# Kernel optimization log

Hardware: AMD Instinct MI355X
Metric: run time of the kernel (lower is better)

Reference implementation:

```python
import math
import jax, jax.numpy as jnp
import numpy as np

DIM = 512
HEADS = 8
B, N = 4, 2048


def _linear_params(key, d_in, d_out):
    # torch nn.Linear default init: U(-1/sqrt(d_in), 1/sqrt(d_in))
    k1, k2 = jax.random.split(key)
    bound = 1.0 / math.sqrt(d_in)
    W = jax.random.uniform(k1, (d_out, d_in), minval=-bound, maxval=bound, dtype=jnp.float32)
    b = jax.random.uniform(k2, (d_out,), minval=-bound, maxval=bound, dtype=jnp.float32)
    return W, b


def setup_inputs() -> dict:
    key = jax.random.key(0)
    kq, kv, km, k1, k2, k3, k4 = jax.random.split(key, 7)
    Q = jax.random.normal(kq, (B, N, DIM), dtype=jnp.float32)
    V = jax.random.normal(kv, (B, N, DIM), dtype=jnp.float32)
    mask = jax.random.bernoulli(km, 0.9, (B, N))  # bool [B, Nk]
    Wq, bq = _linear_params(k1, DIM, DIM)
    Wk, bk = _linear_params(k2, DIM, DIM)
    Wv, bv = _linear_params(k3, DIM, DIM)
    Wo, bo = _linear_params(k4, DIM, DIM)
    return {"Q": Q, "V": V, "mask": mask,
            "Wq": Wq, "bq": bq, "Wk": Wk, "bk": bk,
            "Wv": Wv, "bv": bv, "Wo": Wo, "bo": bo}


def reference(Q, V, mask, Wq, bq, Wk, bk, Wv, bv, Wo, bo):
    Bb, Nq, _ = Q.shape
    dv = Wq.shape[0]
    h = HEADS
    d = dv // h
    q = Q @ Wq.T + bq          # [B, Nq, dv]
    k = V @ Wk.T + bk          # [B, Nk, dv]
    v = V @ Wv.T + bv          # [B, Nk, dv]
    # split heads: torch.cat(split(dim_split, dim=2), dim=0) == head-major stacking
    qh = q.reshape(Bb, Nq, h, d).transpose(2, 0, 1, 3)   # [h, B, Nq, d]
    kh = k.reshape(Bb, -1, h, d).transpose(2, 0, 1, 3)   # [h, B, Nk, d]
    vh = v.reshape(Bb, -1, h, d).transpose(2, 0, 1, 3)   # [h, B, Nk, d]
    # NOTE: original scales by sqrt(Q.shape[-1]) AFTER projection == sqrt(dim_V)
    logits = jnp.einsum('hbqd,hbkd->hbqk', qh, kh) / math.sqrt(dv)
    logits = jnp.where(mask[None, :, None, :], logits, jnp.float32(-100.0))
    A = jax.nn.softmax(logits, axis=-1)
    Oh = qh + jnp.einsum('hbqk,hbkd->hbqd', A, vh)       # residual inside attention
    O = Oh.transpose(1, 2, 0, 3).reshape(Bb, Nq, dv)     # merge heads
    return O + jax.nn.relu(O @ Wo.T + bo)
```

## Files before the change

kernel.cpp:

```cpp
#include <hip/hip_runtime.h>


typedef __attribute__((ext_vector_type(8))) __bf16 bf16x8;
typedef __attribute__((ext_vector_type(4))) float f32x4;

#define DEV static __device__ __forceinline__

constexpr int DIMC = 512;
constexpr int NTOK = 2048;
constexpr int BB   = 4;
constexpr int MTOK = BB * NTOK;
constexpr float SCALE2 = 0.04419417382415922f * 1.4426950408889634f;

DEV unsigned short f2b(float f) {
  unsigned u = __float_as_uint(f);
  u = (u + 0x7FFFu + ((u >> 16) & 1u)) >> 16;
  return (unsigned short)u;
}
DEV float b2f(unsigned short b) { return __uint_as_float(((unsigned)b) << 16); }

DEV unsigned cvtpk(float a, float b) {
  unsigned r;
  asm("v_cvt_pk_bf16_f32 %0, %1, %2" : "=v"(r) : "v"(a), "v"(b));
  return r;
}

DEV bf16x8 pack8(unsigned d0, unsigned d1, unsigned d2, unsigned d3) {
  union { unsigned u[4]; bf16x8 v; } t;
  t.u[0] = d0; t.u[1] = d1; t.u[2] = d2; t.u[3] = d3;
  return t.v;
}

DEV void async_cp16(const void* src, void* dst) {
  __builtin_amdgcn_global_load_lds(
      (const __attribute__((address_space(1))) void*)(src),
      (__attribute__((address_space(3))) void*)(dst), 16, 0, 0);
}

__global__ void cvt_all(const float* __restrict__ Wq, const float* __restrict__ Wk,
                        const float* __restrict__ Wv, const float* __restrict__ Wo,
                        unsigned short* __restrict__ Wqb, unsigned short* __restrict__ Wkb,
                        unsigned short* __restrict__ Wvb, unsigned short* __restrict__ Wob,
                        const unsigned char* __restrict__ mask, int* __restrict__ flag) {
  if (blockIdx.x == 4096) {
    int any = 0;
    for (int i = threadIdx.x; i < BB * NTOK; i += blockDim.x)
      if ((i & 3) == 1 && mask[i]) any = 1;
    if (any) atomicOr(flag, 1);
    return;
  }
  int i = blockIdx.x * blockDim.x + threadIdx.x;
  int wsel = i >> 16, off = i & 65535;
  const float* s = (wsel == 0) ? Wq : (wsel == 1) ? Wk : (wsel == 2) ? Wv : Wo;
  unsigned short* d = (wsel == 0) ? Wqb : (wsel == 1) ? Wkb : (wsel == 2) ? Wvb : Wob;
  float4 v = reinterpret_cast<const float4*>(s)[off];
  ushort4 o;
  o.x = f2b(v.x); o.y = f2b(v.y); o.z = f2b(v.z); o.w = f2b(v.w);
  reinterpret_cast<ushort4*>(d)[off] = o;
}

__global__ __launch_bounds__(256) void proj_gemm(
    const float* __restrict__ Qf, const float* __restrict__ Vf,
    const unsigned short* __restrict__ Wqb, const unsigned short* __restrict__ Wkb,
    const unsigned short* __restrict__ Wvb,
    const float* __restrict__ bq, const float* __restrict__ bk,
    const float* __restrict__ bv,
    unsigned short* __restrict__ qbf, unsigned short* __restrict__ kbf,
    unsigned short* __restrict__ vtb) {
  __shared__ union {
    struct { float A[2][4096]; unsigned short B[2][4096]; } s;
    unsigned short LT[128 * 136];
  } lds;

  const int region = blockIdx.z;
  const float* Af = (region == 0) ? Qf : Vf;
  const unsigned short* W = (region == 0) ? Wqb : (region == 1) ? Wkb : Wvb;
  const float* bias = (region == 0) ? bq : (region == 1) ? bk : bv;

  const int tid = threadIdx.x;
  const int lane = tid & 63;
  const int w = tid >> 6;
  const int r = lane & 15, g = lane >> 4;
  const int rowB = blockIdx.x * 128;
  const int colB = blockIdx.y * 128;
  const int rw = (w >> 1) * 64, cw = (w & 1) * 64;

  auto stageA = [&](float* dst, int kk) {
#pragma unroll
    for (int i = 0; i < 4; ++i) {
      int off = i * 4096 + tid * 16;
      int row = off >> 7;
      int c = ((off >> 4) & 7) ^ (row & 7);
      async_cp16(Af + (size_t)(rowB + row) * DIMC + kk + c * 4, (char*)dst + off);
    }
  };
  auto stageB = [&](unsigned short* dst, int kk) {
#pragma unroll
    for (int i = 0; i < 2; ++i) {
      int off = i * 4096 + tid * 16;
      int row = off >> 6;
      int c = ((off >> 4) & 3) ^ (row & 3);
      async_cp16(W + (size_t)(colB + row) * DIMC + kk + c * 8, (char*)dst + off);
    }
  };

  f32x4 acc[4][4];
#pragma unroll
  for (int i = 0; i < 4; ++i)
#pragma unroll
    for (int j = 0; j < 4; ++j) acc[i][j] = f32x4{0.f, 0.f, 0.f, 0.f};

  stageA(lds.s.A[0], 0);
  stageB(lds.s.B[0], 0);
  __syncthreads();

  int cur = 0;
  for (int kk = 0; kk < DIMC; kk += 32) {
    if (kk + 32 < DIMC) {
      stageA(lds.s.A[cur ^ 1], kk + 32);
      stageB(lds.s.B[cur ^ 1], kk + 32);
    }
    const char* ap = (const char*)lds.s.A[cur];
    const char* bp = (const char*)lds.s.B[cur];
    bf16x8 af[4], bw[4];
#pragma unroll
    for (int i = 0; i < 4; ++i) {
      int row = rw + i * 16 + r;
      f32x4 lo = *reinterpret_cast<const f32x4*>(
          ap + row * 128 + (((2 * g) ^ (row & 7)) << 4));
      f32x4 hi = *reinterpret_cast<const f32x4*>(
          ap + row * 128 + (((2 * g + 1) ^ (row & 7)) << 4));
      af[i] = pack8(cvtpk(lo[0], lo[1]), cvtpk(lo[2], lo[3]),
                    cvtpk(hi[0], hi[1]), cvtpk(hi[2], hi[3]));
    }
#pragma unroll
    for (int j = 0; j < 4; ++j) {
      int row = cw + j * 16 + r;
      bw[j] = *reinterpret_cast<const bf16x8*>(bp + row * 64 + ((g ^ (row & 3)) * 16));
    }
    __builtin_amdgcn_s_setprio(1);
#pragma unroll
    for (int i = 0; i < 4; ++i)
#pragma unroll
      for (int j = 0; j < 4; ++j)
        acc[i][j] = __builtin_amdgcn_mfma_f32_16x16x32_bf16(af[i], bw[j],
                                                            acc[i][j], 0, 0, 0);
    __builtin_amdgcn_s_setprio(0);
    __syncthreads();
    cur ^= 1;
  }

  if (region != 2) {
    const float sc = (region == 1) ? SCALE2 : 1.0f;
    unsigned short* dst = (region == 1) ? kbf : qbf;
#pragma unroll
    for (int i = 0; i < 4; ++i)
#pragma unroll
      for (int j = 0; j < 4; ++j) {
        int n = colB + cw + j * 16 + r;
        float bn = bias[n];
#pragma unroll
        for (int q = 0; q < 4; ++q) {
          int m = rowB + rw + i * 16 + g * 4 + q;
          dst[(size_t)m * DIMC + n] = f2b((acc[i][j][q] + bn) * sc);
        }
      }
  } else {
#pragma unroll
    for (int i = 0; i < 4; ++i)
#pragma unroll
      for (int j = 0; j < 4; ++j) {
        int nl = cw + j * 16 + r;
        float bn = bias[colB + nl];
        int tl = rw + i * 16 + g * 4;
        ushort4 o;
        o.x = f2b(acc[i][j][0] + bn);
        o.y = f2b(acc[i][j][1] + bn);
        o.z = f2b(acc[i][j][2] + bn);
        o.w = f2b(acc[i][j][3] + bn);
        *reinterpret_cast<ushort4*>(&lds.LT[nl * 136 + tl]) = o;
      }
    __syncthreads();
    int bidx = rowB >> 11, t0 = rowB & 2047;
#pragma unroll
    for (int rd = 0; rd < 8; ++rd) {
      int idx = rd * 256 + tid;
      int dv = idx >> 4, ch = idx & 15;
      int gdv = colB + dv, h = gdv >> 6, dd = gdv & 63;
      ushort4 v0 = *reinterpret_cast<const ushort4*>(&lds.LT[dv * 136 + ch * 8]);
      ushort4 v1 = *reinterpret_cast<const ushort4*>(&lds.LT[dv * 136 + ch * 8 + 4]);
      unsigned short* dst = vtb + (size_t)((bidx * 8 + h) * 64 + dd) * NTOK + t0 + ch * 8;
      reinterpret_cast<ushort4*>(dst)[0] = v0;
      reinterpret_cast<ushort4*>(dst)[1] = v1;
    }
  }
}

__global__ __launch_bounds__(256) void out_gemm(
    const float* __restrict__ Of32, const unsigned short* __restrict__ W,
    const float* __restrict__ bias, float* __restrict__ outf) {
  __shared__ struct { float A[2][2048]; unsigned short B[2][4096]; } lds;

  const int tid = threadIdx.x;
  const int lane = tid & 63;
  const int w = tid >> 6;
  const int r = lane & 15, g = lane >> 4;
  const int rowB = blockIdx.x * 64;
  const int colB = blockIdx.y * 128;
  const int rw = (w >> 1) * 32, cw = (w & 1) * 64;

  auto stageA = [&](float* dst, int kk) {
    int off = tid * 16;
#pragma unroll
    for (int i = 0; i < 2; ++i) {
      int o2 = off + i * 4096;
      int row = o2 >> 7;
      int c = ((o2 >> 4) & 7) ^ (row & 7);
      async_cp16(Of32 + (size_t)(rowB + row) * DIMC + kk + c * 4, (char*)dst + o2);
    }
  };
  auto stageB = [&](unsigned short* dst, int kk) {
#pragma unroll
    for (int i = 0; i < 2; ++i) {
      int off = i * 4096 + tid * 16;
      int row = off >> 6;
      int c = ((off >> 4) & 3) ^ (row & 3);
      async_cp16(W + (size_t)(colB + row) * DIMC + kk + c * 8, (char*)dst + off);
    }
  };

  f32x4 acc[2][4];
#pragma unroll
  for (int i = 0; i < 2; ++i)
#pragma unroll
    for (int j = 0; j < 4; ++j) acc[i][j] = f32x4{0.f, 0.f, 0.f, 0.f};

  stageA(lds.A[0], 0);
  stageB(lds.B[0], 0);
  __syncthreads();

  int cur = 0;
  for (int kk = 0; kk < DIMC; kk += 32) {
    if (kk + 32 < DIMC) {
      stageA(lds.A[cur ^ 1], kk + 32);
      stageB(lds.B[cur ^ 1], kk + 32);
    }
    const char* ap = (const char*)lds.A[cur];
    const char* bp = (const char*)lds.B[cur];
    bf16x8 af[2], bw[4];
#pragma unroll
    for (int i = 0; i < 2; ++i) {
      int row = rw + i * 16 + r;
      f32x4 lo = *reinterpret_cast<const f32x4*>(
          ap + row * 128 + (((2 * g) ^ (row & 7)) << 4));
      f32x4 hi = *reinterpret_cast<const f32x4*>(
          ap + row * 128 + (((2 * g + 1) ^ (row & 7)) << 4));
      af[i] = pack8(cvtpk(lo[0], lo[1]), cvtpk(lo[2], lo[3]),
                    cvtpk(hi[0], hi[1]), cvtpk(hi[2], hi[3]));
    }
#pragma unroll
    for (int j = 0; j < 4; ++j) {
      int row = cw + j * 16 + r;
      bw[j] = *reinterpret_cast<const bf16x8*>(bp + row * 64 + ((g ^ (row & 3)) * 16));
    }
    __builtin_amdgcn_s_setprio(1);
#pragma unroll
    for (int i = 0; i < 2; ++i)
#pragma unroll
      for (int j = 0; j < 4; ++j)
        acc[i][j] = __builtin_amdgcn_mfma_f32_16x16x32_bf16(af[i], bw[j],
                                                            acc[i][j], 0, 0, 0);
    __builtin_amdgcn_s_setprio(0);
    __syncthreads();
    cur ^= 1;
  }

#pragma unroll
  for (int i = 0; i < 2; ++i)
#pragma unroll
    for (int j = 0; j < 4; ++j) {
      int n = colB + cw + j * 16 + r;
      float bn = bias[n];
#pragma unroll
      for (int q = 0; q < 4; ++q) {
        int m = rowB + rw + i * 16 + g * 4 + q;
        float val = acc[i][j][q] + bn;
        outf[(size_t)m * DIMC + n] = Of32[(size_t)m * DIMC + n] + fmaxf(val, 0.f);
      }
    }
}

__global__ __launch_bounds__(512, 4) void attn_kernel(
    const unsigned short* __restrict__ qb, const unsigned short* __restrict__ kb,
    const unsigned short* __restrict__ vt, const unsigned char* __restrict__ mask8,
    const int* __restrict__ flagp, float* __restrict__ Of32) {
  __shared__ unsigned short Kt[2][2][64 * 64];
  __shared__ unsigned short Vt[2][2][64 * 64];
  __shared__ float MaskAdd[NTOK];

  const int tid = threadIdx.x;
  const int lane = tid & 63;
  const int w = tid >> 6;
  const int kg = w >> 2;
  const int wq = w & 3;
  const int r = lane & 15, g = lane >> 4;
  const int bh = blockIdx.x, b = bh >> 3, h = bh & 7;
  const int q0 = blockIdx.y * 128 + wq * 32;
  const size_t rowbase = (size_t)b * NTOK;
  const int flag = *flagp;
  const unsigned* mask32 = (const unsigned*)mask8;

  for (int i = tid; i < NTOK; i += 512) {
    unsigned v = flag ? (unsigned)mask8[b * NTOK + i] : mask32[b * NTOK + i];
    MaskAdd[i] = v ? 0.f : -16384.f;
  }

  bf16x8 aq0[2], aq1[2];
#pragma unroll
  for (int ks = 0; ks < 2; ++ks) {
    aq0[ks] = *reinterpret_cast<const bf16x8*>(
        qb + (rowbase + q0 + r) * DIMC + h * 64 + ks * 32 + g * 8);
    aq1[ks] = *reinterpret_cast<const bf16x8*>(
        qb + (rowbase + q0 + 16 + r) * DIMC + h * 64 + ks * 32 + g * 8);
  }

  const unsigned short* kgb = kb + rowbase * DIMC + h * 64;
  const unsigned short* vgb = vt + (size_t)bh * 64 * NTOK;

  auto stageK = [&](int pb, int tile, int kt) {
    int off = tid * 16;
    int row = off >> 7;
    int s16 = ((off >> 4) & 7) ^ (row & 7);
    int ff = row >> 4, gg = (row >> 2) & 3, j = row & 3;
    int tok = 8 * gg + 4 * (ff & 1) + 32 * (ff >> 1) + j;
    async_cp16(kgb + (size_t)(kt + tok) * DIMC + (s16 << 3),
               (char*)&Kt[pb][tile][0] + off);
  };
  auto stageV = [&](int pb, int tile, int kt) {
    int off = tid * 16;
    int row = off >> 7;
    int s16 = ((off >> 4) & 7) ^ (row & 7);
    async_cp16(vgb + (size_t)row * NTOK + kt + (s16 << 3),
               (char*)&Vt[pb][tile][0] + off);
  };
  auto stagePair = [&](int pb, int p) {
    stageK(pb, 0, p * 128);
    stageK(pb, 1, p * 128 + 64);
    stageV(pb, 0, p * 128);
    stageV(pb, 1, p * 128 + 64);
  };

  stagePair(0, 0);
  __syncthreads();

  float lrun0 = 0.f, lrun1 = 0.f;
  f32x4 oacc0[4], oacc1[4];
#pragma unroll
  for (int f = 0; f < 4; ++f) {
    oacc0[f] = f32x4{0.f, 0.f, 0.f, 0.f};
    oacc1[f] = f32x4{0.f, 0.f, 0.f, 0.f};
  }

  const int swz = (r & 7) << 4;

  auto softmax_pa = [&](f32x4 (&s)[4], float& lr, bf16x8 (&pa)[2]) {
#pragma unroll
    for (int f = 0; f < 4; ++f)
#pragma unroll
      for (int j = 0; j < 4; ++j) s[f][j] = __builtin_exp2f(s[f][j]);
    float sf[4];
#pragma unroll
    for (int f = 0; f < 4; ++f)
      sf[f] = (s[f][0] + s[f][1]) + (s[f][2] + s[f][3]);
    lr += (sf[0] + sf[1]) + (sf[2] + sf[3]);
#pragma unroll
    for (int ks = 0; ks < 2; ++ks)
      pa[ks] = pack8(cvtpk(s[2 * ks][0], s[2 * ks][1]),
                     cvtpk(s[2 * ks][2], s[2 * ks][3]),
                     cvtpk(s[2 * ks + 1][0], s[2 * ks + 1][1]),
                     cvtpk(s[2 * ks + 1][2], s[2 * ks + 1][3]));
  };

  int cur = 0;
  for (int p = 0; p < NTOK / 128; ++p) {
    if (p + 1 < NTOK / 128) stagePair(cur ^ 1, p + 1);

    const int kt = p * 128 + kg * 64;

    f32x4 s0[4], s1[4];
#pragma unroll
    for (int f = 0; f < 4; ++f) {
      int tb = kt + 8 * g + 4 * (f & 1) + 32 * (f >> 1);
      f32x4 mc = *reinterpret_cast<const f32x4*>(&MaskAdd[tb]);
      s0[f] = mc;
      s1[f] = mc;
    }
    const unsigned char* kp = (const unsigned char*)&Kt[cur][kg][0];
    __builtin_amdgcn_s_setprio(1);
#pragma unroll
    for (int ks = 0; ks < 2; ++ks)
#pragma unroll
      for (int f = 0; f < 4; ++f) {
        bf16x8 kf = *reinterpret_cast<const bf16x8*>(
            kp + (f * 16 + r) * 128 + ((ks * 64 + g * 16) ^ swz));
        s0[f] = __builtin_amdgcn_mfma_f32_16x16x32_bf16(kf, aq0[ks], s0[f], 0, 0, 0);
        s1[f] = __builtin_amdgcn_mfma_f32_16x16x32_bf16(kf, aq1[ks], s1[f], 0, 0, 0);
      }
    __builtin_amdgcn_s_setprio(0);

    bf16x8 pa0[2], pa1[2];
    softmax_pa(s0, lrun0, pa0);
    softmax_pa(s1, lrun1, pa1);

    const unsigned char* vp = (const unsigned char*)&Vt[cur][kg][0];
    __builtin_amdgcn_s_setprio(1);
#pragma unroll
    for (int ks = 0; ks < 2; ++ks)
#pragma unroll
      for (int f = 0; f < 4; ++f) {
        bf16x8 vf = *reinterpret_cast<const bf16x8*>(
            vp + (f * 16 + r) * 128 + ((ks * 64 + g * 16) ^ swz));
        oacc0[f] = __builtin_amdgcn_mfma_f32_16x16x32_bf16(pa0[ks], vf, oacc0[f], 0, 0, 0);
        oacc1[f] = __builtin_amdgcn_mfma_f32_16x16x32_bf16(pa1[ks], vf, oacc1[f], 0, 0, 0);
      }
    __builtin_amdgcn_s_setprio(0);

    __syncthreads();
    cur ^= 1;
  }

  lrun0 += __shfl_xor(lrun0, 16);
  lrun0 += __shfl_xor(lrun0, 32);
  lrun1 += __shfl_xor(lrun1, 16);
  lrun1 += __shfl_xor(lrun1, 32);

  f32x4* cb4 = (f32x4*)&Kt[0][0][0];
  float* cl = (float*)&Vt[0][0][0];
  if (kg == 1) {
#pragma unroll
    for (int f = 0; f < 4; ++f) {
      cb4[wq * 512 + f * 64 + lane] = oacc0[f];
      cb4[wq * 512 + (4 + f) * 64 + lane] = oacc1[f];
    }
    if (g == 0) {
      cl[wq * 32 + r] = lrun0;
      cl[wq * 32 + 16 + r] = lrun1;
    }
  }
  __syncthreads();
  if (kg == 0) {
#pragma unroll
    for (int f = 0; f < 4; ++f) {
      oacc0[f] += cb4[wq * 512 + f * 64 + lane];
      oacc1[f] += cb4[wq * 512 + (4 + f) * 64 + lane];
    }
    lrun0 += cl[wq * 32 + r];
    lrun1 += cl[wq * 32 + 16 + r];

    auto epilogue = [&](float lr, f32x4 (&oa)[4], int qoff) {
#pragma unroll
      for (int j = 0; j < 4; ++j) {
        float linv = 1.0f / __shfl(lr, (lane & 48) | (g * 4 + j));
        int row = q0 + qoff + g * 4 + j;
#pragma unroll
        for (int f = 0; f < 4; ++f) {
          int col = h * 64 + f * 16 + r;
          size_t idx = (rowbase + row) * DIMC + col;
          Of32[idx] = b2f(qb[idx]) + oa[f][j] * linv;
        }
      }
    };
    epilogue(lrun0, oacc0, 0);
    epilogue(lrun1, oacc1, 16);
  }
}

extern "C" void kernel_launch(void* const* d_in, const int* in_sizes, int n_in,
                              void* d_out, int out_size, void* d_ws, size_t ws_size,
                              hipStream_t stream) {
  const float* Q  = (const float*)d_in[0];
  const float* V  = (const float*)d_in[1];
  const unsigned char* mask = (const unsigned char*)d_in[2];
  const float* Wq = (const float*)d_in[3];
  const float* bq = (const float*)d_in[4];
  const float* Wk = (const float*)d_in[5];
  const float* bk = (const float*)d_in[6];
  const float* Wv = (const float*)d_in[7];
  const float* bv = (const float*)d_in[8];
  const float* Wo = (const float*)d_in[9];
  const float* bo = (const float*)d_in[10];

  char* ws = (char*)d_ws;
  size_t off = 0;
  auto alloc = [&](size_t bytes) -> void* {
    void* p = ws + off;
    off += (bytes + 255) & ~(size_t)255;
    return p;
  };
  int* flag = (int*)alloc(4);
  unsigned short* Wqb = (unsigned short*)alloc((size_t)DIMC * DIMC * 2);
  unsigned short* Wkb = (unsigned short*)alloc((size_t)DIMC * DIMC * 2);
  unsigned short* Wvb = (unsigned short*)alloc((size_t)DIMC * DIMC * 2);
  unsigned short* Wob = (unsigned short*)alloc((size_t)DIMC * DIMC * 2);
  unsigned short* qbf = (unsigned short*)alloc((size_t)MTOK * DIMC * 2);
  unsigned short* kbf = (unsigned short*)alloc((size_t)MTOK * DIMC * 2);
  unsigned short* vtb = (unsigned short*)alloc((size_t)MTOK * DIMC * 2);
  float* Of32 = (float*)alloc((size_t)MTOK * DIMC * 4);

  hipMemsetAsync(flag, 0, 4, stream);

  cvt_all<<<4097, 256, 0, stream>>>(Wq, Wk, Wv, Wo, Wqb, Wkb, Wvb, Wob,
                                    mask, flag);

  proj_gemm<<<dim3(64, 4, 3), 256, 0, stream>>>(
      Q, V, Wqb, Wkb, Wvb, bq, bk, bv, qbf, kbf, vtb);

  attn_kernel<<<dim3(BB * 8, NTOK / 128), 512, 0, stream>>>(
      qbf, kbf, vtb, mask, flag, Of32);

  out_gemm<<<dim3(128, 4), 256, 0, stream>>>(
      Of32, Wob, bo, (float*)d_out);
}
```

Measured before the change: 117.6 us.

## Halve attention block to 4 waves, each computing 64 query rows

The attention kernel now launches 256 threads per block instead of 512. Each wave handles four 16-row query subtiles instead of two, so every K/V fragment read from LDS is reused across 64 query rows, and each thread issues two async copies per tile. This cuts LDS traffic per MFMA and sync overhead, but roughly doubles accumulator and score registers per wave and lowers the waves available per block to hide latency.

```diff
diff --git a/kernel.cpp b/kernel.cpp
--- a/kernel.cpp
+++ b/kernel.cpp
@@ -290,7 +290,7 @@
     }
 }
 
-__global__ __launch_bounds__(512, 4) void attn_kernel(
+__global__ __launch_bounds__(256, 2) void attn_kernel(
     const unsigned short* __restrict__ qb, const unsigned short* __restrict__ kb,
     const unsigned short* __restrict__ vt, const unsigned char* __restrict__ mask8,
     const int* __restrict__ flagp, float* __restrict__ Of32) {
@@ -301,47 +301,52 @@
   const int tid = threadIdx.x;
   const int lane = tid & 63;
   const int w = tid >> 6;
-  const int kg = w >> 2;
-  const int wq = w & 3;
+  const int kg = w >> 1;
+  const int wq = w & 1;
   const int r = lane & 15, g = lane >> 4;
   const int bh = blockIdx.x, b = bh >> 3, h = bh & 7;
-  const int q0 = blockIdx.y * 128 + wq * 32;
+  const int q0 = blockIdx.y * 128 + wq * 64;
   const size_t rowbase = (size_t)b * NTOK;
   const int flag = *flagp;
   const unsigned* mask32 = (const unsigned*)mask8;
 
-  for (int i = tid; i < NTOK; i += 512) {
+  for (int i = tid; i < NTOK; i += 256) {
     unsigned v = flag ? (unsigned)mask8[b * NTOK + i] : mask32[b * NTOK + i];
     MaskAdd[i] = v ? 0.f : -16384.f;
   }
 
-  bf16x8 aq0[2], aq1[2];
-#pragma unroll
-  for (int ks = 0; ks < 2; ++ks) {
-    aq0[ks] = *reinterpret_cast<const bf16x8*>(
-        qb + (rowbase + q0 + r) * DIMC + h * 64 + ks * 32 + g * 8);
-    aq1[ks] = *reinterpret_cast<const bf16x8*>(
-        qb + (rowbase + q0 + 16 + r) * DIMC + h * 64 + ks * 32 + g * 8);
-  }
+  bf16x8 aq[4][2];
+#pragma unroll
+  for (int sub = 0; sub < 4; ++sub)
+#pragma unroll
+    for (int ks = 0; ks < 2; ++ks)
+      aq[sub][ks] = *reinterpret_cast<const bf16x8*>(
+          qb + (rowbase + q0 + sub * 16 + r) * DIMC + h * 64 + ks * 32 + g * 8);
 
   const unsigned short* kgb = kb + rowbase * DIMC + h * 64;
   const unsigned short* vgb = vt + (size_t)bh * 64 * NTOK;
 
   auto stageK = [&](int pb, int tile, int kt) {
-    int off = tid * 16;
-    int row = off >> 7;
-    int s16 = ((off >> 4) & 7) ^ (row & 7);
-    int ff = row >> 4, gg = (row >> 2) & 3, j = row & 3;
-    int tok = 8 * gg + 4 * (ff & 1) + 32 * (ff >> 1) + j;
-    async_cp16(kgb + (size_t)(kt + tok) * DIMC + (s16 << 3),
-               (char*)&Kt[pb][tile][0] + off);
+#pragma unroll
+    for (int i = 0; i < 2; ++i) {
+      int off = i * 4096 + tid * 16;
+      int row = off >> 7;
+      int s16 = ((off >> 4) & 7) ^ (row & 7);
+      int ff = row >> 4, gg = (row >> 2) & 3, j = row & 3;
+      int tok = 8 * gg + 4 * (ff & 1) + 32 * (ff >> 1) + j;
+      async_cp16(kgb + (size_t)(kt + tok) * DIMC + (s16 << 3),
+                 (char*)&Kt[pb][tile][0] + off);
+    }
   };
   auto stageV = [&](int pb, int tile, int kt) {
-    int off = tid * 16;
-    int row = off >> 7;
-    int s16 = ((off >> 4) & 7) ^ (row & 7);
-    async_cp16(vgb + (size_t)row * NTOK + kt + (s16 << 3),
-               (char*)&Vt[pb][tile][0] + off);
+#pragma unroll
+    for (int i = 0; i < 2; ++i) {
+      int off = i * 4096 + tid * 16;
+      int row = off >> 7;
+      int s16 = ((off >> 4) & 7) ^ (row & 7);
+      async_cp16(vgb + (size_t)row * NTOK + kt + (s16 << 3),
+                 (char*)&Vt[pb][tile][0] + off);
+    }
   };
   auto stagePair = [&](int pb, int p) {
     stageK(pb, 0, p * 128);
@@ -353,33 +358,14 @@
   stagePair(0, 0);
   __syncthreads();
 
-  float lrun0 = 0.f, lrun1 = 0.f;
-  f32x4 oacc0[4], oacc1[4];
-#pragma unroll
-  for (int f = 0; f < 4; ++f) {
-    oacc0[f] = f32x4{0.f, 0.f, 0.f, 0.f};
-    oacc1[f] = f32x4{0.f, 0.f, 0.f, 0.f};
-  }
+  float lrun[4] = {0.f, 0.f, 0.f, 0.f};
+  f32x4 oacc[4][4];
+#pragma unroll
+  for (int sub = 0; sub < 4; ++sub)
+#pragma unroll
+    for (int f = 0; f < 4; ++f) oacc[sub][f] = f32x4{0.f, 0.f, 0.f, 0.f};
 
   const int swz = (r & 7) << 4;
-
-  auto softmax_pa = [&](f32x4 (&s)[4], float& lr, bf16x8 (&pa)[2]) {
-#pragma unroll
-    for (int f = 0; f < 4; ++f)
-#pragma unroll
-      for (int j = 0; j < 4; ++j) s[f][j] = __builtin_exp2f(s[f][j]);
-    float sf[4];
-#pragma unroll
-    for (int f = 0; f < 4; ++f)
-      sf[f] = (s[f][0] + s[f][1]) + (s[f][2] + s[f][3]);
-    lr += (sf[0] + sf[1]) + (sf[2] + sf[3]);
-#pragma unroll
-    for (int ks = 0; ks < 2; ++ks)
-      pa[ks] = pack8(cvtpk(s[2 * ks][0], s[2 * ks][1]),
-                     cvtpk(s[2 * ks][2], s[2 * ks][3]),
-                     cvtpk(s[2 * ks + 1][0], s[2 * ks + 1][1]),
-                     cvtpk(s[2 * ks + 1][2], s[2 * ks + 1][3]));
-  };
 
   int cur = 0;
   for (int p = 0; p < NTOK / 128; ++p) {
@@ -387,13 +373,13 @@
 
     const int kt = p * 128 + kg * 64;
 
-    f32x4 s0[4], s1[4];
+    f32x4 s[4][4];
 #pragma unroll
     for (int f = 0; f < 4; ++f) {
       int tb = kt + 8 * g + 4 * (f & 1) + 32 * (f >> 1);
       f32x4 mc = *reinterpret_cast<const f32x4*>(&MaskAdd[tb]);
-      s0[f] = mc;
-      s1[f] = mc;
+#pragma unroll
+      for (int sub = 0; sub < 4; ++sub) s[sub][f] = mc;
     }
     const unsigned char* kp = (const unsigned char*)&Kt[cur][kg][0];
     __builtin_amdgcn_s_setprio(1);
@@ -403,14 +389,32 @@
       for (int f = 0; f < 4; ++f) {
         bf16x8 kf = *reinterpret_cast<const bf16x8*>(
             kp + (f * 16 + r) * 128 + ((ks * 64 + g * 16) ^ swz));
-        s0[f] = __builtin_amdgcn_mfma_f32_16x16x32_bf16(kf, aq0[ks], s0[f], 0, 0, 0);
-        s1[f] = __builtin_amdgcn_mfma_f32_16x16x32_bf16(kf, aq1[ks], s1[f], 0, 0, 0);
+#pragma unroll
+        for (int sub = 0; sub < 4; ++sub)
+          s[sub][f] = __builtin_amdgcn_mfma_f32_16x16x32_bf16(
+              kf, aq[sub][ks], s[sub][f], 0, 0, 0);
       }
     __builtin_amdgcn_s_setprio(0);
 
-    bf16x8 pa0[2], pa1[2];
-    softmax_pa(s0, lrun0, pa0);
-    softmax_pa(s1, lrun1, pa1);
+    bf16x8 pa[4][2];
+#pragma unroll
+    for (int sub = 0; sub < 4; ++sub) {
+#pragma unroll
+      for (int f = 0; f < 4; ++f)
+#pragma unroll
+        for (int j = 0; j < 4; ++j) s[sub][f][j] = __builtin_exp2f(s[sub][f][j]);
+      float sf[4];
+#pragma unroll
+      for (int f = 0; f < 4; ++f)
+        sf[f] = (s[sub][f][0] + s[sub][f][1]) + (s[sub][f][2] + s[sub][f][3]);
+      lrun[sub] += (sf[0] + sf[1]) + (sf[2] + sf[3]);
+#pragma unroll
+      for (int ks = 0; ks < 2; ++ks)
+        pa[sub][ks] = pack8(cvtpk(s[sub][2 * ks][0], s[sub][2 * ks][1]),
+                            cvtpk(s[sub][2 * ks][2], s[sub][2 * ks][3]),
+                            cvtpk(s[sub][2 * ks + 1][0], s[sub][2 * ks + 1][1]),
+                            cvtpk(s[sub][2 * ks + 1][2], s[sub][2 * ks + 1][3]));
+    }
 
     const unsigned char* vp = (const unsigned char*)&Vt[cur][kg][0];
     __builtin_amdgcn_s_setprio(1);
@@ -420,8 +424,10 @@
       for (int f = 0; f < 4; ++f) {
         bf16x8 vf = *reinterpret_cast<const bf16x8*>(
             vp + (f * 16 + r) * 128 + ((ks * 64 + g * 16) ^ swz));
-        oacc0[f] = __builtin_amdgcn_mfma_f32_16x16x32_bf16(pa0[ks], vf, oacc0[f], 0, 0, 0);
-        oacc1[f] = __builtin_amdgcn_mfma_f32_16x16x32_bf16(pa1[ks], vf, oacc1[f], 0, 0, 0);
+#pragma unroll
+        for (int sub = 0; sub < 4; ++sub)
+          oacc[sub][f] = __builtin_amdgcn_mfma_f32_16x16x32_bf16(
+              pa[sub][ks], vf, oacc[sub][f], 0, 0, 0);
       }
     __builtin_amdgcn_s_setprio(0);
 
@@ -429,49 +435,48 @@
     cur ^= 1;
   }
 
-  lrun0 += __shfl_xor(lrun0, 16);
-  lrun0 += __shfl_xor(lrun0, 32);
-  lrun1 += __shfl_xor(lrun1, 16);
-  lrun1 += __shfl_xor(lrun1, 32);
+#pragma unroll
+  for (int sub = 0; sub < 4; ++sub) {
+    lrun[sub] += __shfl_xor(lrun[sub], 16);
+    lrun[sub] += __shfl_xor(lrun[sub], 32);
+  }
 
   f32x4* cb4 = (f32x4*)&Kt[0][0][0];
   float* cl = (float*)&Vt[0][0][0];
   if (kg == 1) {
 #pragma unroll
-    for (int f = 0; f < 4; ++f) {
-      cb4[wq * 512 + f * 64 + lane] = oacc0[f];
-      cb4[wq * 512 + (4 + f) * 64 + lane] = oacc1[f];
-    }
+    for (int sub = 0; sub < 4; ++sub)
+#pragma unroll
+      for (int f = 0; f < 4; ++f)
+        cb4[((wq * 4 + sub) * 4 + f) * 64 + lane] = oacc[sub][f];
     if (g == 0) {
-      cl[wq * 32 + r] = lrun0;
-      cl[wq * 32 + 16 + r] = lrun1;
+#pragma unroll
+      for (int sub = 0; sub < 4; ++sub) cl[(wq * 4 + sub) * 16 + r] = lrun[sub];
     }
   }
   __syncthreads();
   if (kg == 0) {
 #pragma unroll
-    for (int f = 0; f < 4; ++f) {
-      oacc0[f] += cb4[wq * 512 + f * 64 + lane];
-      oacc1[f] += cb4[wq * 512 + (4 + f) * 64 + lane];
-    }
-    lrun0 += cl[wq * 32 + r];
-    lrun1 += cl[wq * 32 + 16 + r];
-
-    auto epilogue = [&](float lr, f32x4 (&oa)[4], int qoff) {
+    for (int sub = 0; sub < 4; ++sub) {
+#pragma unroll
+      for (int f = 0; f < 4; ++f)
+        oacc[sub][f] += cb4[((wq * 4 + sub) * 4 + f) * 64 + lane];
+      lrun[sub] += cl[(wq * 4 + sub) * 16 + r];
+    }
+
+#pragma unroll
+    for (int sub = 0; sub < 4; ++sub)
 #pragma unroll
       for (int j = 0; j < 4; ++j) {
-        float linv = 1.0f / __shfl(lr, (lane & 48) | (g * 4 + j));
-        int row = q0 + qoff + g * 4 + j;
+        float linv = 1.0f / __shfl(lrun[sub], (lane & 48) | (g * 4 + j));
+        int row = q0 + sub * 16 + g * 4 + j;
 #pragma unroll
         for (int f = 0; f < 4; ++f) {
           int col = h * 64 + f * 16 + r;
           size_t idx = (rowbase + row) * DIMC + col;
-          Of32[idx] = b2f(qb[idx]) + oa[f][j] * linv;
+          Of32[idx] = b2f(qb[idx]) + oacc[sub][f][j] * linv;
         }
       }
-    };
-    epilogue(lrun0, oacc0, 0);
-    epilogue(lrun1, oacc1, 16);
   }
 }
 
@@ -515,7 +520,7 @@
   proj_gemm<<<dim3(64, 4, 3), 256, 0, stream>>>(
       Q, V, Wqb, Wkb, Wvb, bq, bk, bv, qbf, kbf, vtb);
 
-  attn_kernel<<<dim3(BB * 8, NTOK / 128), 512, 0, stream>>>(
+  attn_kernel<<<dim3(BB * 8, NTOK / 128), 256, 0, stream>>>(
       qbf, kbf, vtb, mask, flag, Of32);
 
   out_gemm<<<dim3(128, 4), 256, 0, stream>>>(
```

After: 120.4 us. +2.4%, slower.

## Fuse K/V projections sharing the V tile and store attention output as bf16

Applied to the files above, without the earlier changes.

The projection GEMM now computes K and V together in one block, so the fp32 V activation tile is loaded and converted to bf16 once instead of twice. The grid shrinks from three regions to two. The attention output intermediate is now stored in bf16 instead of fp32, which halves its write and read traffic and removes the fp32-to-bf16 conversion in the output GEMM's A path. In exchange, the fused K/V blocks carry twice the accumulators and extra LDS, which may lower occupancy and leave the grid unbalanced. The residual added in the final output also loses precision from the bf16 rounding.

```diff
diff --git a/kernel.cpp b/kernel.cpp
--- a/kernel.cpp
+++ b/kernel.cpp
@@ -68,14 +68,12 @@
     unsigned short* __restrict__ qbf, unsigned short* __restrict__ kbf,
     unsigned short* __restrict__ vtb) {
   __shared__ union {
-    struct { float A[2][4096]; unsigned short B[2][4096]; } s;
+    struct { float A[2][4096]; unsigned short Bk[2][4096]; unsigned short Bv[2][4096]; } s;
     unsigned short LT[128 * 136];
   } lds;
 
   const int region = blockIdx.z;
   const float* Af = (region == 0) ? Qf : Vf;
-  const unsigned short* W = (region == 0) ? Wqb : (region == 1) ? Wkb : Wvb;
-  const float* bias = (region == 0) ? bq : (region == 1) ? bk : bv;
 
   const int tid = threadIdx.x;
   const int lane = tid & 63;
@@ -94,7 +92,7 @@
       async_cp16(Af + (size_t)(rowB + row) * DIMC + kk + c * 4, (char*)dst + off);
     }
   };
-  auto stageB = [&](unsigned short* dst, int kk) {
+  auto stageB = [&](unsigned short* dst, const unsigned short* W, int kk) {
 #pragma unroll
     for (int i = 0; i < 2; ++i) {
       int off = i * 4096 + tid * 16;
@@ -104,25 +102,31 @@
     }
   };
 
-  f32x4 acc[4][4];
+  f32x4 acck[4][4], accv[4][4];
 #pragma unroll
   for (int i = 0; i < 4; ++i)
 #pragma unroll
-    for (int j = 0; j < 4; ++j) acc[i][j] = f32x4{0.f, 0.f, 0.f, 0.f};
+    for (int j = 0; j < 4; ++j) {
+      acck[i][j] = f32x4{0.f, 0.f, 0.f, 0.f};
+      accv[i][j] = f32x4{0.f, 0.f, 0.f, 0.f};
+    }
 
   stageA(lds.s.A[0], 0);
-  stageB(lds.s.B[0], 0);
+  stageB(lds.s.Bk[0], (region == 0) ? Wqb : Wkb, 0);
+  if (region == 1) stageB(lds.s.Bv[0], Wvb, 0);
   __syncthreads();
 
   int cur = 0;
   for (int kk = 0; kk < DIMC; kk += 32) {
     if (kk + 32 < DIMC) {
       stageA(lds.s.A[cur ^ 1], kk + 32);
-      stageB(lds.s.B[cur ^ 1], kk + 32);
+      stageB(lds.s.Bk[cur ^ 1], (region == 0) ? Wqb : Wkb, kk + 32);
+      if (region == 1) stageB(lds.s.Bv[cur ^ 1], Wvb, kk + 32);
     }
     const char* ap = (const char*)lds.s.A[cur];
-    const char* bp = (const char*)lds.s.B[cur];
-    bf16x8 af[4], bw[4];
+    const char* bpk = (const char*)lds.s.Bk[cur];
+    const char* bpv = (const char*)lds.s.Bv[cur];
+    bf16x8 af[4], bwk[4];
 #pragma unroll
     for (int i = 0; i < 4; ++i) {
       int row = rw + i * 16 + r;
@@ -136,48 +140,74 @@
 #pragma unroll
     for (int j = 0; j < 4; ++j) {
       int row = cw + j * 16 + r;
-      bw[j] = *reinterpret_cast<const bf16x8*>(bp + row * 64 + ((g ^ (row & 3)) * 16));
+      bwk[j] = *reinterpret_cast<const bf16x8*>(bpk + row * 64 + ((g ^ (row & 3)) * 16));
     }
     __builtin_amdgcn_s_setprio(1);
 #pragma unroll
     for (int i = 0; i < 4; ++i)
 #pragma unroll
       for (int j = 0; j < 4; ++j)
-        acc[i][j] = __builtin_amdgcn_mfma_f32_16x16x32_bf16(af[i], bw[j],
-                                                            acc[i][j], 0, 0, 0);
+        acck[i][j] = __builtin_amdgcn_mfma_f32_16x16x32_bf16(af[i], bwk[j],
+                                                             acck[i][j], 0, 0, 0);
     __builtin_amdgcn_s_setprio(0);
+    if (region == 1) {
+      bf16x8 bwv[4];
+#pragma unroll
+      for (int j = 0; j < 4; ++j) {
+        int row = cw + j * 16 + r;
+        bwv[j] = *reinterpret_cast<const bf16x8*>(bpv + row * 64 + ((g ^ (row & 3)) * 16));
+      }
+      __builtin_amdgcn_s_setprio(1);
+#pragma unroll
+      for (int i = 0; i < 4; ++i)
+#pragma unroll
+        for (int j = 0; j < 4; ++j)
+          accv[i][j] = __builtin_amdgcn_mfma_f32_16x16x32_bf16(af[i], bwv[j],
+                                                               accv[i][j], 0, 0, 0);
+      __builtin_amdgcn_s_setprio(0);
+    }
     __syncthreads();
     cur ^= 1;
   }
 
-  if (region != 2) {
-    const float sc = (region == 1) ? SCALE2 : 1.0f;
-    unsigned short* dst = (region == 1) ? kbf : qbf;
+  if (region == 0) {
 #pragma unroll
     for (int i = 0; i < 4; ++i)
 #pragma unroll
       for (int j = 0; j < 4; ++j) {
         int n = colB + cw + j * 16 + r;
-        float bn = bias[n];
+        float bn = bq[n];
 #pragma unroll
         for (int q = 0; q < 4; ++q) {
           int m = rowB + rw + i * 16 + g * 4 + q;
-          dst[(size_t)m * DIMC + n] = f2b((acc[i][j][q] + bn) * sc);
+          qbf[(size_t)m * DIMC + n] = f2b(acck[i][j][q] + bn);
         }
       }
   } else {
+#pragma unroll
+    for (int i = 0; i < 4; ++i)
+#pragma unroll
+      for (int j = 0; j < 4; ++j) {
+        int n = colB + cw + j * 16 + r;
+        float bn = bk[n];
+#pragma unroll
+        for (int q = 0; q < 4; ++q) {
+          int m = rowB + rw + i * 16 + g * 4 + q;
+          kbf[(size_t)m * DIMC + n] = f2b((acck[i][j][q] + bn) * SCALE2);
+        }
+      }
 #pragma unroll
     for (int i = 0; i < 4; ++i)
 #pragma unroll
       for (int j = 0; j < 4; ++j) {
         int nl = cw + j * 16 + r;
-        float bn = bias[colB + nl];
+        float bn = bv[colB + nl];
         int tl = rw + i * 16 + g * 4;
         ushort4 o;
-        o.x = f2b(acc[i][j][0] + bn);
-        o.y = f2b(acc[i][j][1] + bn);
-        o.z = f2b(acc[i][j][2] + bn);
-        o.w = f2b(acc[i][j][3] + bn);
+        o.x = f2b(accv[i][j][0] + bn);
+        o.y = f2b(accv[i][j][1] + bn);
+        o.z = f2b(accv[i][j][2] + bn);
+        o.w = f2b(accv[i][j][3] + bn);
         *reinterpret_cast<ushort4*>(&lds.LT[nl * 136 + tl]) = o;
       }
     __syncthreads();
@@ -197,9 +227,9 @@
 }
 
 __global__ __launch_bounds__(256) void out_gemm(
-    const float* __restrict__ Of32, const unsigned short* __restrict__ W,
+    const unsigned short* __restrict__ Obf, const unsigned short* __restrict__ W,
     const float* __restrict__ bias, float* __restrict__ outf) {
-  __shared__ struct { float A[2][2048]; unsigned short B[2][4096]; } lds;
+  __shared__ struct { unsigned short A[2][2048]; unsigned short B[2][4096]; } lds;
 
   const int tid = threadIdx.x;
   const int lane = tid & 63;
@@ -209,15 +239,11 @@
   const int colB = blockIdx.y * 128;
   const int rw = (w >> 1) * 32, cw = (w & 1) * 64;
 
-  auto stageA = [&](float* dst, int kk) {
+  auto stageA = [&](unsigned short* dst, int kk) {
     int off = tid * 16;
-#pragma unroll
-    for (int i = 0; i < 2; ++i) {
-      int o2 = off + i * 4096;
-      int row = o2 >> 7;
-      int c = ((o2 >> 4) & 7) ^ (row & 7);
-      async_cp16(Of32 + (size_t)(rowB + row) * DIMC + kk + c * 4, (char*)dst + o2);
-    }
+    int row = off >> 6;
+    int c = ((off >> 4) & 3) ^ (row & 3);
+    async_cp16(Obf + (size_t)(rowB + row) * DIMC + kk + c * 8, (char*)dst + off);
   };
   auto stageB = [&](unsigned short* dst, int kk) {
 #pragma unroll
@@ -251,12 +277,7 @@
 #pragma unroll
     for (int i = 0; i < 2; ++i) {
       int row = rw + i * 16 + r;
-      f32x4 lo = *reinterpret_cast<const f32x4*>(
-          ap + row * 128 + (((2 * g) ^ (row & 7)) << 4));
-      f32x4 hi = *reinterpret_cast<const f32x4*>(
-          ap + row * 128 + (((2 * g + 1) ^ (row & 7)) << 4));
-      af[i] = pack8(cvtpk(lo[0], lo[1]), cvtpk(lo[2], lo[3]),
-                    cvtpk(hi[0], hi[1]), cvtpk(hi[2], hi[3]));
+      af[i] = *reinterpret_cast<const bf16x8*>(ap + row * 64 + ((g ^ (row & 3)) * 16));
     }
 #pragma unroll
     for (int j = 0; j < 4; ++j) {
@@ -285,7 +306,8 @@
       for (int q = 0; q < 4; ++q) {
         int m = rowB + rw + i * 16 + g * 4 + q;
         float val = acc[i][j][q] + bn;
-        outf[(size_t)m * DIMC + n] = Of32[(size_t)m * DIMC + n] + fmaxf(val, 0.f);
+        outf[(size_t)m * DIMC + n] =
+            b2f(Obf[(size_t)m * DIMC + n]) + fmaxf(val, 0.f);
       }
     }
 }
@@ -293,7 +315,7 @@
 __global__ __launch_bounds__(512, 4) void attn_kernel(
     const unsigned short* __restrict__ qb, const unsigned short* __restrict__ kb,
     const unsigned short* __restrict__ vt, const unsigned char* __restrict__ mask8,
-    const int* __restrict__ flagp, float* __restrict__ Of32) {
+    const int* __restrict__ flagp, unsigned short* __restrict__ Obf) {
   __shared__ unsigned short Kt[2][2][64 * 64];
   __shared__ unsigned short Vt[2][2][64 * 64];
   __shared__ float MaskAdd[NTOK];
@@ -466,7 +488,7 @@
         for (int f = 0; f < 4; ++f) {
           int col = h * 64 + f * 16 + r;
           size_t idx = (rowbase + row) * DIMC + col;
-          Of32[idx] = b2f(qb[idx]) + oa[f][j] * linv;
+          Obf[idx] = f2b(b2f(qb[idx]) + oa[f][j] * linv);
         }
       }
     };
@@ -505,19 +527,19 @@
   unsigned short* qbf = (unsigned short*)alloc((size_t)MTOK * DIMC * 2);
   unsigned short* kbf = (unsigned short*)alloc((size_t)MTOK * DIMC * 2);
   unsigned short* vtb = (unsigned short*)alloc((size_t)MTOK * DIMC * 2);
-  float* Of32 = (float*)alloc((size_t)MTOK * DIMC * 4);
+  unsigned short* Obf = (unsigned short*)alloc((size_t)MTOK * DIMC * 2);
 
   hipMemsetAsync(flag, 0, 4, stream);
 
   cvt_all<<<4097, 256, 0, stream>>>(Wq, Wk, Wv, Wo, Wqb, Wkb, Wvb, Wob,
                                     mask, flag);
 
-  proj_gemm<<<dim3(64, 4, 3), 256, 0, stream>>>(
+  proj_gemm<<<dim3(64, 4, 2), 256, 0, stream>>>(
       Q, V, Wqb, Wkb, Wvb, bq, bk, bv, qbf, kbf, vtb);
 
   attn_kernel<<<dim3(BB * 8, NTOK / 128), 512, 0, stream>>>(
-      qbf, kbf, vtb, mask, flag, Of32);
+      qbf, kbf, vtb, mask, flag, Obf);
 
   out_gemm<<<dim3(128, 4), 256, 0, stream>>>(
-      Of32, Wob, bo, (float*)d_out);
-}
+      Obf, Wob, bo, (float*)d_out);
+}
```

Measured after the change: 117.6 us, median of 2. About the same (+0.0%).

## Fuse weight bf16 conversion into GEMMs and store attention output as bf16

Applied to the files above, without the earlier changes.

Drops the separate weight-conversion kernel: the projection and output GEMMs now stage fp32 weights into LDS and convert them to bf16 in registers, as already done for activations. The mask-flag scan moves into one block of the projection kernel. The attention output is stored as bf16 instead of fp32, halving that intermediate's write and read traffic. The cost is doubled LDS footprint and global traffic for weight tiles, extra conversion instructions per k-step, and lower precision on the residual path into the output.

```diff
diff --git a/kernel.cpp b/kernel.cpp
--- a/kernel.cpp
+++ b/kernel.cpp
@@ -37,44 +37,23 @@
       (__attribute__((address_space(3))) void*)(dst), 16, 0, 0);
 }
 
-__global__ void cvt_all(const float* __restrict__ Wq, const float* __restrict__ Wk,
-                        const float* __restrict__ Wv, const float* __restrict__ Wo,
-                        unsigned short* __restrict__ Wqb, unsigned short* __restrict__ Wkb,
-                        unsigned short* __restrict__ Wvb, unsigned short* __restrict__ Wob,
-                        const unsigned char* __restrict__ mask, int* __restrict__ flag) {
-  if (blockIdx.x == 4096) {
-    int any = 0;
-    for (int i = threadIdx.x; i < BB * NTOK; i += blockDim.x)
-      if ((i & 3) == 1 && mask[i]) any = 1;
-    if (any) atomicOr(flag, 1);
-    return;
-  }
-  int i = blockIdx.x * blockDim.x + threadIdx.x;
-  int wsel = i >> 16, off = i & 65535;
-  const float* s = (wsel == 0) ? Wq : (wsel == 1) ? Wk : (wsel == 2) ? Wv : Wo;
-  unsigned short* d = (wsel == 0) ? Wqb : (wsel == 1) ? Wkb : (wsel == 2) ? Wvb : Wob;
-  float4 v = reinterpret_cast<const float4*>(s)[off];
-  ushort4 o;
-  o.x = f2b(v.x); o.y = f2b(v.y); o.z = f2b(v.z); o.w = f2b(v.w);
-  reinterpret_cast<ushort4*>(d)[off] = o;
-}
-
 __global__ __launch_bounds__(256) void proj_gemm(
     const float* __restrict__ Qf, const float* __restrict__ Vf,
-    const unsigned short* __restrict__ Wqb, const unsigned short* __restrict__ Wkb,
-    const unsigned short* __restrict__ Wvb,
+    const float* __restrict__ Wq, const float* __restrict__ Wk,
+    const float* __restrict__ Wv,
     const float* __restrict__ bq, const float* __restrict__ bk,
     const float* __restrict__ bv,
     unsigned short* __restrict__ qbf, unsigned short* __restrict__ kbf,
-    unsigned short* __restrict__ vtb) {
+    unsigned short* __restrict__ vtb,
+    const unsigned char* __restrict__ mask, int* __restrict__ flag) {
   __shared__ union {
-    struct { float A[2][4096]; unsigned short B[2][4096]; } s;
+    struct { float A[2][4096]; float B[2][4096]; } s;
     unsigned short LT[128 * 136];
   } lds;
 
   const int region = blockIdx.z;
   const float* Af = (region == 0) ? Qf : Vf;
-  const unsigned short* W = (region == 0) ? Wqb : (region == 1) ? Wkb : Wvb;
+  const float* W = (region == 0) ? Wq : (region == 1) ? Wk : Wv;
   const float* bias = (region == 0) ? bq : (region == 1) ? bk : bv;
 
   const int tid = threadIdx.x;
@@ -85,22 +64,20 @@
   const int colB = blockIdx.y * 128;
   const int rw = (w >> 1) * 64, cw = (w & 1) * 64;
 
-  auto stageA = [&](float* dst, int kk) {
+  if (region == 0 && blockIdx.x == 0 && blockIdx.y == 0) {
+    int any = 0;
+    for (int i = tid; i < BB * NTOK; i += 256)
+      if ((i & 3) == 1 && mask[i]) any = 1;
+    if (any) atomicOr(flag, 1);
+  }
+
+  auto stageT = [&](float* dst, const float* src, int kk) {
 #pragma unroll
     for (int i = 0; i < 4; ++i) {
       int off = i * 4096 + tid * 16;
       int row = off >> 7;
       int c = ((off >> 4) & 7) ^ (row & 7);
-      async_cp16(Af + (size_t)(rowB + row) * DIMC + kk + c * 4, (char*)dst + off);
-    }
-  };
-  auto stageB = [&](unsigned short* dst, int kk) {
-#pragma unroll
-    for (int i = 0; i < 2; ++i) {
-      int off = i * 4096 + tid * 16;
-      int row = off >> 6;
-      int c = ((off >> 4) & 3) ^ (row & 3);
-      async_cp16(W + (size_t)(colB + row) * DIMC + kk + c * 8, (char*)dst + off);
+      async_cp16(src + (size_t)row * DIMC + kk + c * 4, (char*)dst + off);
     }
   };
 
@@ -110,15 +87,15 @@
 #pragma unroll
     for (int j = 0; j < 4; ++j) acc[i][j] = f32x4{0.f, 0.f, 0.f, 0.f};
 
-  stageA(lds.s.A[0], 0);
-  stageB(lds.s.B[0], 0);
+  stageT(lds.s.A[0], Af + (size_t)rowB * DIMC, 0);
+  stageT(lds.s.B[0], W + (size_t)colB * DIMC, 0);
   __syncthreads();
 
   int cur = 0;
   for (int kk = 0; kk < DIMC; kk += 32) {
     if (kk + 32 < DIMC) {
-      stageA(lds.s.A[cur ^ 1], kk + 32);
-      stageB(lds.s.B[cur ^ 1], kk + 32);
+      stageT(lds.s.A[cur ^ 1], Af + (size_t)rowB * DIMC, kk + 32);
+      stageT(lds.s.B[cur ^ 1], W + (size_t)colB * DIMC, kk + 32);
     }
     const char* ap = (const char*)lds.s.A[cur];
     const char* bp = (const char*)lds.s.B[cur];
@@ -136,7 +113,12 @@
 #pragma unroll
     for (int j = 0; j < 4; ++j) {
       int row = cw + j * 16 + r;
-      bw[j] = *reinterpret_cast<const bf16x8*>(bp + row * 64 + ((g ^ (row & 3)) * 16));
+      f32x4 lo = *reinterpret_cast<const f32x4*>(
+          bp + row * 128 + (((2 * g) ^ (row & 7)) << 4));
+      f32x4 hi = *reinterpret_cast<const f32x4*>(
+          bp + row * 128 + (((2 * g + 1) ^ (row & 7)) << 4));
+      bw[j] = pack8(cvtpk(lo[0], lo[1]), cvtpk(lo[2], lo[3]),
+                    cvtpk(hi[0], hi[1]), cvtpk(hi[2], hi[3]));
     }
     __builtin_amdgcn_s_setprio(1);
 #pragma unroll
@@ -197,9 +179,9 @@
 }
 
 __global__ __launch_bounds__(256) void out_gemm(
-    const float* __restrict__ Of32, const unsigned short* __restrict__ W,
+    const unsigned short* __restrict__ Obf, const float* __restrict__ W,
     const float* __restrict__ bias, float* __restrict__ outf) {
-  __shared__ struct { float A[2][2048]; unsigned short B[2][4096]; } lds;
+  __shared__ struct { unsigned short A[2][2048]; float B[2][4096]; } lds;
 
   const int tid = threadIdx.x;
   const int lane = tid & 63;
@@ -209,23 +191,19 @@
   const int colB = blockIdx.y * 128;
   const int rw = (w >> 1) * 32, cw = (w & 1) * 64;
 
-  auto stageA = [&](float* dst, int kk) {
+  auto stageA = [&](unsigned short* dst, int kk) {
     int off = tid * 16;
-#pragma unroll
-    for (int i = 0; i < 2; ++i) {
-      int o2 = off + i * 4096;
-      int row = o2 >> 7;
-      int c = ((o2 >> 4) & 7) ^ (row & 7);
-      async_cp16(Of32 + (size_t)(rowB + row) * DIMC + kk + c * 4, (char*)dst + o2);
-    }
-  };
-  auto stageB = [&](unsigned short* dst, int kk) {
-#pragma unroll
-    for (int i = 0; i < 2; ++i) {
+    int row = off >> 6;
+    int c = ((off >> 4) & 3) ^ (row & 3);
+    async_cp16(Obf + (size_t)(rowB + row) * DIMC + kk + c * 8, (char*)dst + off);
+  };
+  auto stageB = [&](float* dst, int kk) {
+#pragma unroll
+    for (int i = 0; i < 4; ++i) {
       int off = i * 4096 + tid * 16;
-      int row = off >> 6;
-      int c = ((off >> 4) & 3) ^ (row & 3);
-      async_cp16(W + (size_t)(colB + row) * DIMC + kk + c * 8, (char*)dst + off);
+      int row = off >> 7;
+      int c = ((off >> 4) & 7) ^ (row & 7);
+      async_cp16(W + (size_t)(colB + row) * DIMC + kk + c * 4, (char*)dst + off);
     }
   };
 
@@ -251,17 +229,17 @@
 #pragma unroll
     for (int i = 0; i < 2; ++i) {
       int row = rw + i * 16 + r;
-      f32x4 lo = *reinterpret_cast<const f32x4*>(
-          ap + row * 128 + (((2 * g) ^ (row & 7)) << 4));
-      f32x4 hi = *reinterpret_cast<const f32x4*>(
-          ap + row * 128 + (((2 * g + 1) ^ (row & 7)) << 4));
-      af[i] = pack8(cvtpk(lo[0], lo[1]), cvtpk(lo[2], lo[3]),
-                    cvtpk(hi[0], hi[1]), cvtpk(hi[2], hi[3]));
+      af[i] = *reinterpret_cast<const bf16x8*>(ap + row * 64 + ((g ^ (row & 3)) * 16));
     }
 #pragma unroll
     for (int j = 0; j < 4; ++j) {
       int row = cw + j * 16 + r;
-      bw[j] = *reinterpret_cast<const bf16x8*>(bp + row * 64 + ((g ^ (row & 3)) * 16));
+      f32x4 lo = *reinterpret_cast<const f32x4*>(
+          bp + row * 128 + (((2 * g) ^ (row & 7)) << 4));
+      f32x4 hi = *reinterpret_cast<const f32x4*>(
+          bp + row * 128 + (((2 * g + 1) ^ (row & 7)) << 4));
+      bw[j] = pack8(cvtpk(lo[0], lo[1]), cvtpk(lo[2], lo[3]),
+                    cvtpk(hi[0], hi[1]), cvtpk(hi[2], hi[3]));
     }
     __builtin_amdgcn_s_setprio(1);
 #pragma unroll
@@ -285,7 +263,8 @@
       for (int q = 0; q < 4; ++q) {
         int m = rowB + rw + i * 16 + g * 4 + q;
         float val = acc[i][j][q] + bn;
-        outf[(size_t)m * DIMC + n] = Of32[(size_t)m * DIMC + n] + fmaxf(val, 0.f);
+        outf[(size_t)m * DIMC + n] =
+            b2f(Obf[(size_t)m * DIMC + n]) + fmaxf(val, 0.f);
       }
     }
 }
@@ -293,7 +272,7 @@
 __global__ __launch_bounds__(512, 4) void attn_kernel(
     const unsigned short* __restrict__ qb, const unsigned short* __restrict__ kb,
     const unsigned short* __restrict__ vt, const unsigned char* __restrict__ mask8,
-    const int* __restrict__ flagp, float* __restrict__ Of32) {
+    const int* __restrict__ flagp, unsigned short* __restrict__ Obf) {
   __shared__ unsigned short Kt[2][2][64 * 64];
   __shared__ unsigned short Vt[2][2][64 * 64];
   __shared__ float MaskAdd[NTOK];
@@ -466,7 +445,7 @@
         for (int f = 0; f < 4; ++f) {
           int col = h * 64 + f * 16 + r;
           size_t idx = (rowbase + row) * DIMC + col;
-          Of32[idx] = b2f(qb[idx]) + oa[f][j] * linv;
+          Obf[idx] = f2b(b2f(qb[idx]) + oa[f][j] * linv);
         }
       }
     };
@@ -498,26 +477,19 @@
     return p;
   };
   int* flag = (int*)alloc(4);
-  unsigned short* Wqb = (unsigned short*)alloc((size_t)DIMC * DIMC * 2);
-  unsigned short* Wkb = (unsigned short*)alloc((size_t)DIMC * DIMC * 2);
-  unsigned short* Wvb = (unsigned short*)alloc((size_t)DIMC * DIMC * 2);
-  unsigned short* Wob = (unsigned short*)alloc((size_t)DIMC * DIMC * 2);
   unsigned short* qbf = (unsigned short*)alloc((size_t)MTOK * DIMC * 2);
   unsigned short* kbf = (unsigned short*)alloc((size_t)MTOK * DIMC * 2);
   unsigned short* vtb = (unsigned short*)alloc((size_t)MTOK * DIMC * 2);
-  float* Of32 = (float*)alloc((size_t)MTOK * DIMC * 4);
+  unsigned short* Obf = (unsigned short*)alloc((size_t)MTOK * DIMC * 2);
 
   hipMemsetAsync(flag, 0, 4, stream);
 
-  cvt_all<<<4097, 256, 0, stream>>>(Wq, Wk, Wv, Wo, Wqb, Wkb, Wvb, Wob,
-                                    mask, flag);
-
   proj_gemm<<<dim3(64, 4, 3), 256, 0, stream>>>(
-      Q, V, Wqb, Wkb, Wvb, bq, bk, bv, qbf, kbf, vtb);
+      Q, V, Wq, Wk, Wv, bq, bk, bv, qbf, kbf, vtb, mask, flag);
 
   attn_kernel<<<dim3(BB * 8, NTOK / 128), 512, 0, stream>>>(
-      qbf, kbf, vtb, mask, flag, Of32);
+      qbf, kbf, vtb, mask, flag, Obf);
 
   out_gemm<<<dim3(128, 4), 256, 0, stream>>>(
-      Of32, Wob, bo, (float*)d_out);
-}
+      Obf, Wo, bo, (float*)d_out);
+}
```

Measured after the change: 112.2 us, median of 2. -4.6%, faster.
